# Optimization experiments

Measured on AMD Instinct MI355X. Metric: run time of the kernel, lower is better.

## Reference

```python
import jax, jax.numpy as jnp
import numpy as np

ROI_SIZE = 14  # hard-coded in the torch module


def _bilinear(feature, x, y):
    """feature: [B,C,H,W]; x, y: arbitrary (matching) shape S of sample coords.
    Returns [B, C, *S]. Matches torch code: corner indices are clamped BEFORE
    the interpolation weights are computed from them."""
    H, W = feature.shape[-2:]
    y1 = jnp.clip(jnp.floor(y).astype(jnp.int32), 0, H - 1)
    y2 = jnp.clip(jnp.floor(y).astype(jnp.int32) + 1, 0, H - 1)
    x1 = jnp.clip(jnp.floor(x).astype(jnp.int32), 0, W - 1)
    x2 = jnp.clip(jnp.floor(x).astype(jnp.int32) + 1, 0, W - 1)
    wx_lo = x - x1  # weight toward x2 column
    wx_hi = x2 - x  # weight toward x1 column
    wy_lo = y - y1
    wy_hi = y2 - y
    p = feature[:, :, y1, x1] * wx_hi + feature[:, :, y1, x2] * wx_lo
    q = feature[:, :, y2, x1] * wx_hi + feature[:, :, y2, x2] * wx_lo
    return p * wy_hi + q * wy_lo


def setup_inputs() -> dict:
    key = jax.random.key(0)
    kf, k1, k2, k3, k4 = jax.random.split(key, 5)
    B, C, H, W, R = 1, 256, 200, 320, 128
    feature = jax.random.normal(kf, (B, C, H, W), dtype=jnp.float32)
    y1 = jax.random.uniform(k1, (R,), minval=0.0, maxval=H * 0.5)
    x1 = jax.random.uniform(k2, (R,), minval=0.0, maxval=W * 0.5)
    hh = jax.random.uniform(k3, (R,), minval=8.0, maxval=H * 0.45)
    ww = jax.random.uniform(k4, (R,), minval=8.0, maxval=W * 0.45)
    rois = jnp.stack([y1, x1, y1 + hh, x1 + ww], axis=-1).astype(jnp.float32)
    return {"feature": feature, "rois": rois}


def reference(feature, rois):
    R = rois.shape[0]
    B, C, H, W = feature.shape
    sh = (rois[:, 2] - rois[:, 0]) / ROI_SIZE  # [R] bin height stride
    sw = (rois[:, 3] - rois[:, 1]) / ROI_SIZE  # [R] bin width stride
    m = jnp.arange(ROI_SIZE, dtype=rois.dtype)
    y_base = rois[:, 0:1] + sh[:, None] * m  # [R, M]
    x_base = rois[:, 1:2] + sw[:, None] * m  # [R, N]
    frac = jnp.array([1.0 / 3.0, 2.0 / 3.0], dtype=rois.dtype)
    ys = y_base[:, :, None] + sh[:, None, None] * frac  # [R, M, 2]
    xs = x_base[:, :, None] + sw[:, None, None] * frac  # [R, N, 2]
    # all 4 (y, x) sample-point combos per bin -> [R, M, N, 2, 2]
    yy = jnp.broadcast_to(ys[:, :, None, :, None], (R, ROI_SIZE, ROI_SIZE, 2, 2))
    xx = jnp.broadcast_to(xs[:, None, :, None, :], (R, ROI_SIZE, ROI_SIZE, 2, 2))
    samples = _bilinear(feature, xx, yy)  # [B, C, R, M, N, 2, 2]
    # Faithful to torch.max(tensor) with NO dim: global max over B, C, R and
    # the 4 sample points, giving one scalar per bin (m, n).
    bin_max = jnp.max(samples, axis=(0, 1, 2, 5, 6))  # [M, N]
    return jnp.broadcast_to(bin_max, (R, C, ROI_SIZE, ROI_SIZE))
```

## Files before the change

kernel.cpp:

```cpp
#include <hip/hip_runtime.h>
#include <float.h>

#define CC 256
#define HH 200
#define WW 320
#define HW (HH * WW)
#define MM 14
#define CG 4
#define CPB (CC / CG)
#define KPW 16

__global__ void roi_init(float* __restrict__ binmax) {
    int t = blockIdx.x * blockDim.x + threadIdx.x;
    if (t < MM * MM) binmax[t] = -FLT_MAX;
}

__device__ inline void atomicMaxF(float* addr, float val) {
    if (val >= 0.0f) {
        atomicMax((int*)addr, __float_as_int(val));
    } else {
        atomicMin((unsigned int*)addr, __float_as_uint(val));
    }
}

__global__ __launch_bounds__(256, 8) void roi_reduce(
    const float* __restrict__ feature,
    const float* __restrict__ rois,
    float* __restrict__ binmax)
{
    const int bid = blockIdx.x;
    const int cg  = bid & (CG - 1);
    const int rm  = bid >> 2;
    const int m   = rm % MM;
    const int r   = rm / MM;
    const int tid = threadIdx.x;
    const int w    = tid >> 6;
    const int lane = tid & 63;
    const int s    = (lane < 56) ? lane : 55;
    const int cbase = cg * CPB + w * KPW;

    const float ry1 = rois[r * 4 + 0];
    const float rx1 = rois[r * 4 + 1];
    const float ry2 = rois[r * 4 + 2];
    const float rx2 = rois[r * 4 + 3];
    const float sh = (ry2 - ry1) * (1.0f / 14.0f);
    const float sw = (rx2 - rx1) * (1.0f / 14.0f);
    const float f13 = 1.0f / 3.0f, f23 = 2.0f / 3.0f;

    const int ii  = s / 28;
    const int rem = s % 28;
    const int nn  = rem >> 1;
    const int jj  = rem & 1;

    const float y = ry1 + sh * (float)m + sh * (ii ? f23 : f13);
    const float x = rx1 + sw * (float)nn + sw * (jj ? f23 : f13);

    const int y1c = min(max((int)floorf(y), 0), HH - 1);
    const int y2c = min(max((int)floorf(y) + 1, 0), HH - 1);
    const int x1c = min(max((int)floorf(x), 0), WW - 1);
    const int x2c = min(max((int)floorf(x) + 1, 0), WW - 1);
    const float wylo = y - (float)y1c, wyhi = (float)y2c - y;
    const float wxlo = x - (float)x1c, wxhi = (float)x2c - x;
    const bool csel = (x2c == x1c);

    typedef float f2v __attribute__((ext_vector_type(2)));
    typedef f2v __attribute__((aligned(4))) f2u;

    const float* pA = feature + (size_t)cbase * HW + y1c * WW + x1c;
    const float* pB = feature + (size_t)cbase * HW + y2c * WW + x1c;

    float lmax = -FLT_MAX;

    #pragma unroll 4
    for (int kk = 0; kk < KPW; ++kk) {
        f2v a = *(const f2u*)pA;
        f2v b = *(const f2u*)pB;
        pA += HW;
        pB += HW;
        float ax2 = csel ? a.x : a.y;
        float bx2 = csel ? b.x : b.y;
        float p = a.x * wxhi + ax2 * wxlo;
        float q = b.x * wxhi + bx2 * wxlo;
        lmax = fmaxf(lmax, p * wyhi + q * wylo);
    }

    __shared__ float pmax[224];
    if (lane < 56) pmax[w * 56 + s] = lmax;
    __syncthreads();
    if (tid < MM) {
        float v = -FLT_MAX;
        #pragma unroll
        for (int c4 = 0; c4 < 4; ++c4) {
            const float* pw = &pmax[c4 * 56 + tid * 2];
            v = fmaxf(v, fmaxf(fmaxf(pw[0], pw[1]), fmaxf(pw[28], pw[29])));
        }
        atomicMaxF(&binmax[m * MM + tid], v);
    }
}

__global__ __launch_bounds__(256) void roi_bcast(
    const float* __restrict__ binmax, float4* __restrict__ out, int total4)
{
    __shared__ float4 b4[49];
    int t = threadIdx.x;
    if (t < 49) b4[t] = ((const float4*)binmax)[t];
    __syncthreads();
    const int stride = gridDim.x * 256;
    for (int idx = blockIdx.x * 256 + t; idx < total4; idx += stride)
        out[idx] = b4[idx % 49];
}

extern "C" void kernel_launch(void* const* d_in, const int* in_sizes, int n_in,
                              void* d_out, int out_size, void* d_ws, size_t ws_size,
                              hipStream_t stream) {
    const float* feature = (const float*)d_in[0];
    const float* rois    = (const float*)d_in[1];
    float* binmax = (float*)d_ws;
    float* out    = (float*)d_out;

    const int R = in_sizes[1] / 4;

    roi_init<<<1, 256, 0, stream>>>(binmax);
    roi_reduce<<<R * MM * CG, 256, 0, stream>>>(feature, rois, binmax);

    const int total4 = out_size / 4;
    int nb = (total4 + 255) / 256;
    if (nb > 2048) nb = 2048;
    roi_bcast<<<nb, 256, 0, stream>>>(binmax, (float4*)out, total4);
}
```

Baseline: 139.5 us.

## Cover both x-samples per lane with one 4-wide load when ROI bins are narrow

When the bin width is at most six pixels, each lane now handles both horizontal sample points of a bin. It reads a single float4 span per row that covers both samples' corner columns, and the lanes split channels into two halves. This roughly halves the number of global load instructions per output value and shares loaded data between the two x-samples. The cost is more FMAs and a second code path with a different shared-memory reduction layout. The original path is kept for wider ROIs.

```diff
diff --git a/kernel.cpp b/kernel.cpp
--- a/kernel.cpp
+++ b/kernel.cpp
@@ -36,7 +36,6 @@
     const int tid = threadIdx.x;
     const int w    = tid >> 6;
     const int lane = tid & 63;
-    const int s    = (lane < 56) ? lane : 55;
     const int cbase = cg * CPB + w * KPW;
 
     const float ry1 = rois[r * 4 + 0];
@@ -47,52 +46,118 @@
     const float sw = (rx2 - rx1) * (1.0f / 14.0f);
     const float f13 = 1.0f / 3.0f, f23 = 2.0f / 3.0f;
 
-    const int ii  = s / 28;
-    const int rem = s % 28;
-    const int nn  = rem >> 1;
-    const int jj  = rem & 1;
+    const bool fastp = (sw <= 6.0f);
 
-    const float y = ry1 + sh * (float)m + sh * (ii ? f23 : f13);
-    const float x = rx1 + sw * (float)nn + sw * (jj ? f23 : f13);
-
-    const int y1c = min(max((int)floorf(y), 0), HH - 1);
-    const int y2c = min(max((int)floorf(y) + 1, 0), HH - 1);
-    const int x1c = min(max((int)floorf(x), 0), WW - 1);
-    const int x2c = min(max((int)floorf(x) + 1, 0), WW - 1);
-    const float wylo = y - (float)y1c, wyhi = (float)y2c - y;
-    const float wxlo = x - (float)x1c, wxhi = (float)x2c - x;
-    const bool csel = (x2c == x1c);
-
+    typedef float f4v __attribute__((ext_vector_type(4)));
+    typedef f4v __attribute__((aligned(4))) f4u;
     typedef float f2v __attribute__((ext_vector_type(2)));
     typedef f2v __attribute__((aligned(4))) f2u;
 
-    const float* pA = feature + (size_t)cbase * HW + y1c * WW + x1c;
-    const float* pB = feature + (size_t)cbase * HW + y2c * WW + x1c;
-
     float lmax = -FLT_MAX;
 
-    #pragma unroll 4
-    for (int kk = 0; kk < KPW; ++kk) {
-        f2v a = *(const f2u*)pA;
-        f2v b = *(const f2u*)pB;
-        pA += HW;
-        pB += HW;
-        float ax2 = csel ? a.x : a.y;
-        float bx2 = csel ? b.x : b.y;
-        float p = a.x * wxhi + ax2 * wxlo;
-        float q = b.x * wxhi + bx2 * wxlo;
-        lmax = fmaxf(lmax, p * wyhi + q * wylo);
+    if (fastp) {
+        if (lane < 56) {
+            const int half = lane / 28;
+            const int u    = lane % 28;
+            const int ii   = u / 14;
+            const int nn   = u % 14;
+
+            const float y = ry1 + sh * (float)m + sh * (ii ? f23 : f13);
+            const int y1c = min(max((int)floorf(y), 0), HH - 1);
+            const int y2c = min(max((int)floorf(y) + 1, 0), HH - 1);
+            const float wylo = y - (float)y1c, wyhi = (float)y2c - y;
+
+            const float x0 = rx1 + sw * (float)nn + sw * f13;
+            const float x1 = rx1 + sw * (float)nn + sw * f23;
+            const int x1c0 = min(max((int)floorf(x0), 0), WW - 1);
+            const int x2c0 = min(max((int)floorf(x0) + 1, 0), WW - 1);
+            const int x1c1 = min(max((int)floorf(x1), 0), WW - 1);
+            const int x2c1 = min(max((int)floorf(x1) + 1, 0), WW - 1);
+            const float wxlo0 = x0 - (float)x1c0, wxhi0 = (float)x2c0 - x0;
+            const float wxlo1 = x1 - (float)x1c1, wxhi1 = (float)x2c1 - x1;
+
+            const int base = min(x1c0, WW - 4);
+            int o1 = x1c1 - base;
+            o1 = min(max(o1, 0), 2);
+
+            f4v wj1;
+            wj1.x = (o1 == 0) ? wxhi1 : 0.0f;
+            wj1.y = (o1 == 0) ? wxlo1 : ((o1 == 1) ? wxhi1 : 0.0f);
+            wj1.z = (o1 == 1) ? wxlo1 : ((o1 == 2) ? wxhi1 : 0.0f);
+            wj1.w = (o1 == 2) ? wxlo1 : 0.0f;
+
+            const float* p1 = feature + ((size_t)(cbase + half)) * HW + y1c * WW + base;
+            const float* p2 = feature + ((size_t)(cbase + half)) * HW + y2c * WW + base;
+
+            #pragma unroll 4
+            for (int it = 0; it < 8; ++it) {
+                f4v a4 = *(const f4u*)p1;
+                f4v b4 = *(const f4u*)p2;
+                p1 += 2 * HW;
+                p2 += 2 * HW;
+                float pa0 = a4.x * wxhi0 + a4.y * wxlo0;
+                float pb0 = b4.x * wxhi0 + b4.y * wxlo0;
+                float s0  = pa0 * wyhi + pb0 * wylo;
+                float pa1 = a4.x * wj1.x + a4.y * wj1.y + a4.z * wj1.z + a4.w * wj1.w;
+                float pb1 = b4.x * wj1.x + b4.y * wj1.y + b4.z * wj1.z + b4.w * wj1.w;
+                float s1  = pa1 * wyhi + pb1 * wylo;
+                lmax = fmaxf(lmax, fmaxf(s0, s1));
+            }
+        }
+    } else {
+        if (lane < 56) {
+            const int s   = lane;
+            const int ii  = s / 28;
+            const int rem = s % 28;
+            const int nn  = rem >> 1;
+            const int jj  = rem & 1;
+
+            const float y = ry1 + sh * (float)m + sh * (ii ? f23 : f13);
+            const float x = rx1 + sw * (float)nn + sw * (jj ? f23 : f13);
+
+            const int y1c = min(max((int)floorf(y), 0), HH - 1);
+            const int y2c = min(max((int)floorf(y) + 1, 0), HH - 1);
+            const int x1c = min(max((int)floorf(x), 0), WW - 1);
+            const int x2c = min(max((int)floorf(x) + 1, 0), WW - 1);
+            const float wylo = y - (float)y1c, wyhi = (float)y2c - y;
+            const float wxlo = x - (float)x1c, wxhi = (float)x2c - x;
+            const bool csel = (x2c == x1c);
+
+            const float* pA = feature + (size_t)cbase * HW + y1c * WW + x1c;
+            const float* pB = feature + (size_t)cbase * HW + y2c * WW + x1c;
+
+            #pragma unroll 4
+            for (int kk = 0; kk < KPW; ++kk) {
+                f2v a = *(const f2u*)pA;
+                f2v b = *(const f2u*)pB;
+                pA += HW;
+                pB += HW;
+                float ax2 = csel ? a.x : a.y;
+                float bx2 = csel ? b.x : b.y;
+                float p = a.x * wxhi + ax2 * wxlo;
+                float q = b.x * wxhi + bx2 * wxlo;
+                lmax = fmaxf(lmax, p * wyhi + q * wylo);
+            }
+        }
     }
 
     __shared__ float pmax[224];
-    if (lane < 56) pmax[w * 56 + s] = lmax;
+    if (lane < 56) pmax[w * 56 + lane] = lmax;
     __syncthreads();
     if (tid < MM) {
         float v = -FLT_MAX;
-        #pragma unroll
-        for (int c4 = 0; c4 < 4; ++c4) {
-            const float* pw = &pmax[c4 * 56 + tid * 2];
-            v = fmaxf(v, fmaxf(fmaxf(pw[0], pw[1]), fmaxf(pw[28], pw[29])));
+        if (fastp) {
+            #pragma unroll
+            for (int c4 = 0; c4 < 4; ++c4) {
+                const float* pw = &pmax[c4 * 56 + tid];
+                v = fmaxf(v, fmaxf(fmaxf(pw[0], pw[14]), fmaxf(pw[28], pw[42])));
+            }
+        } else {
+            #pragma unroll
+            for (int c4 = 0; c4 < 4; ++c4) {
+                const float* pw = &pmax[c4 * 56 + tid * 2];
+                v = fmaxf(v, fmaxf(fmaxf(pw[0], pw[1]), fmaxf(pw[28], pw[29])));
+            }
         }
         atomicMaxF(&binmax[m * MM + tid], v);
     }
```

Result: no change. 138.7 us (-0.5%).
